# Kernel tuning notes

Hardware: AMD Instinct MI355X
Metric: run time of the kernel (lower is better)

The kernel has to match this reference:

```python
import jax, jax.numpy as jnp
import numpy as np
import math

B, S, D = 2, 2048, 1024
H, KV, HD = 16, 4, 64
N_REP = H // KV
ROPE_THETA = 1.0e6


def _rope_tables(seq_len, head_dim, theta):
    inv_freq = 1.0 / (theta ** (np.arange(0, head_dim, 2, dtype=np.float32) / head_dim))
    t = np.arange(seq_len, dtype=np.float32)
    freqs = np.outer(t, inv_freq)                      # [S, HD/2]
    emb = np.concatenate([freqs, freqs], axis=-1)      # [S, HD]
    return jnp.asarray(np.cos(emb)), jnp.asarray(np.sin(emb))


def setup_inputs() -> dict:
    key = jax.random.key(0)
    ks = jax.random.split(key, 6)
    cos, sin = _rope_tables(S, HD, ROPE_THETA)
    scale = 0.02
    return {
        "x": jax.random.normal(ks[0], (B, S, D), dtype=jnp.float32),
        "cos": cos,
        "sin": sin,
        "Wq": jax.random.normal(ks[1], (D, H * HD), dtype=jnp.float32) * scale,
        "Wk": jax.random.normal(ks[2], (D, KV * HD), dtype=jnp.float32) * scale,
        "Wv": jax.random.normal(ks[3], (D, KV * HD), dtype=jnp.float32) * scale,
        "Wo": jax.random.normal(ks[4], (H * HD, D), dtype=jnp.float32) * scale,
    }


def _rotate_half(u):
    u1, u2 = u[..., : HD // 2], u[..., HD // 2 :]
    return jnp.concatenate([-u2, u1], axis=-1)


def reference(x, cos, sin, Wq, Wk, Wv, Wo):
    bsz, seq_len, _ = x.shape
    q = (x @ Wq).reshape(bsz, seq_len, H, HD)   # [B,S,H,HD]
    k = (x @ Wk).reshape(bsz, seq_len, KV, HD)  # [B,S,KV,HD]
    v = (x @ Wv).reshape(bsz, seq_len, KV, HD)

    # RoPE: cos/sin [S,HD] broadcast over batch and heads (unsqueeze_dim=1)
    c = cos[:seq_len][None, :, None, :]
    s = sin[:seq_len][None, :, None, :]
    q = q * c + _rotate_half(q) * s
    k = k * c + _rotate_half(k) * s

    # repeat_kv: expand KV heads groupwise to H heads
    k = jnp.repeat(k, N_REP, axis=2)  # [B,S,H,HD]
    v = jnp.repeat(v, N_REP, axis=2)

    q = q.transpose(0, 2, 1, 3)  # [B,H,S,HD]
    k = k.transpose(0, 2, 1, 3)
    v = v.transpose(0, 2, 1, 3)

    scores = jnp.einsum("bhqd,bhkd->bhqk", q, k) / math.sqrt(HD)
    causal = jnp.tril(jnp.ones((seq_len, seq_len), dtype=bool))
    scores = jnp.where(causal[None, None], scores, jnp.finfo(jnp.float32).min)
    probs = jax.nn.softmax(scores.astype(jnp.float32), axis=-1).astype(x.dtype)

    out = jnp.einsum("bhqk,bhkd->bhqd", probs, v)        # [B,H,S,HD]
    out = out.transpose(0, 2, 1, 3).reshape(bsz, seq_len, H * HD)
    return out @ Wo
```

## Files before the change

kernel.cpp:

```cpp
#include <hip/hip_runtime.h>

#define SS 2048
#define NH 16
#define NKV 4
#define HD 64

typedef __bf16 bf16;
typedef __bf16 bf16x8 __attribute__((ext_vector_type(8)));
typedef float f32x4 __attribute__((ext_vector_type(4)));

#define SM_SCALE 0.18033688011f

__device__ __forceinline__ void gl_lds16(const bf16* g, bf16* l) {
    __builtin_amdgcn_global_load_lds((const __attribute__((address_space(1))) void*)g,
                                     (__attribute__((address_space(3))) void*)l, 16, 0, 0);
}

__global__ __launch_bounds__(256) void prep_kernel(
    const float* __restrict__ Wq, const float* __restrict__ Wk,
    const float* __restrict__ Wv, const float* __restrict__ Wo,
    bf16* __restrict__ wqkv_t, bf16* __restrict__ wo_t)
{
    const int blk = blockIdx.x;
    const int tid = threadIdx.x;
    const float* W; bf16* Wt; int N, n0, k0;
    if (blk < 256)      { W = Wq; Wt = wqkv_t;                       N = 1024; n0 = (blk & 15) * 64;         k0 = (blk >> 4) * 64; }
    else if (blk < 320) { W = Wk; Wt = wqkv_t + (size_t)1024 * 1024; N = 256;  n0 = ((blk - 256) & 3) * 64;  k0 = ((blk - 256) >> 2) * 64; }
    else if (blk < 384) { W = Wv; Wt = wqkv_t + (size_t)1280 * 1024; N = 256;  n0 = ((blk - 320) & 3) * 64;  k0 = ((blk - 320) >> 2) * 64; }
    else                { W = Wo; Wt = wo_t;                         N = 1024; n0 = ((blk - 384) & 15) * 64; k0 = ((blk - 384) >> 4) * 64; }

    __shared__ float Ts[64][65];
    const int c = tid & 63, rr = tid >> 6;
    #pragma unroll
    for (int i = 0; i < 16; ++i) {
        const int kk = i * 4 + rr;
        Ts[kk][c] = W[(size_t)(k0 + kk) * N + n0 + c];
    }
    __syncthreads();
    #pragma unroll
    for (int i = 0; i < 16; ++i) {
        const int nn = i * 4 + rr;
        Wt[(size_t)(n0 + nn) * 1024 + k0 + c] = (bf16)Ts[c][nn];
    }
}

template<int EPI>
__global__ __launch_bounds__(256) void gemm_bt_kernel(
    const bf16* __restrict__ A, const float* __restrict__ Af,
    const bf16* __restrict__ Bt, float* __restrict__ C,
    const float* __restrict__ cosp, const float* __restrict__ sinp,
    bf16* __restrict__ qo, bf16* __restrict__ ko, bf16* __restrict__ vto,
    int M, int N, int K)
{
    __shared__ bf16 As[64 * 64];
    __shared__ bf16 Bs[128 * 64];
    const int m0 = blockIdx.x * 64, n0 = blockIdx.y * 128;
    const int tid = threadIdx.x;
    const int w = tid >> 6, lane = tid & 63, g = lane >> 4, li = lane & 15;
    const int wm = w >> 1, wn = w & 1;

    f32x4 acc[2][4];
    const f32x4 z = {0.f, 0.f, 0.f, 0.f};
    #pragma unroll
    for (int i = 0; i < 2; ++i)
        #pragma unroll
        for (int j = 0; j < 4; ++j) acc[i][j] = z;

    const int srow = tid >> 3;
    const int schunk = ((tid & 7) ^ (srow & 7)) * 8;
    const bf16* pB0 = Bt + (size_t)(n0 + srow) * K + schunk;
    const bf16* pB1 = Bt + (size_t)(n0 + 32 + srow) * K + schunk;
    const bf16* pB2 = Bt + (size_t)(n0 + 64 + srow) * K + schunk;
    const bf16* pB3 = Bt + (size_t)(n0 + 96 + srow) * K + schunk;
    bf16* lB0 = Bs + (size_t)w * 512;
    bf16* lB1 = Bs + 2048 + (size_t)w * 512;
    bf16* lB2 = Bs + 4096 + (size_t)w * 512;
    bf16* lB3 = Bs + 6144 + (size_t)w * 512;
    const bf16* pA0 = (EPI == 0) ? A + (size_t)(m0 + srow) * K + schunk : nullptr;
    const bf16* pA1 = (EPI == 0) ? A + (size_t)(m0 + 32 + srow) * K + schunk : nullptr;
    bf16* lA0 = As + (size_t)w * 512;
    bf16* lA1 = As + 2048 + (size_t)w * 512;

    for (int kk = 0; kk < K; kk += 64) {
        __syncthreads();
        if (EPI == 0) {
            gl_lds16(pA0 + kk, lA0);
            gl_lds16(pA1 + kk, lA1);
        } else {
            #pragma unroll
            for (int s = 0; s < 2; ++s) {
                const float* src = Af + (size_t)(m0 + s * 32 + srow) * K + kk + (tid & 7) * 8;
                const float4 v0 = *(const float4*)src;
                const float4 v1 = *(const float4*)(src + 4);
                bf16x8 t8;
                t8[0] = (bf16)v0.x; t8[1] = (bf16)v0.y; t8[2] = (bf16)v0.z; t8[3] = (bf16)v0.w;
                t8[4] = (bf16)v1.x; t8[5] = (bf16)v1.y; t8[6] = (bf16)v1.z; t8[7] = (bf16)v1.w;
                *(bf16x8*)&As[(s * 32 + srow) * 64 + schunk] = t8;
            }
        }
        gl_lds16(pB0 + kk, lB0);
        gl_lds16(pB1 + kk, lB1);
        gl_lds16(pB2 + kk, lB2);
        gl_lds16(pB3 + kk, lB3);
        __syncthreads();
        #pragma unroll
        for (int t = 0; t < 2; ++t) {
            const int phys = ((t * 4 + g) ^ (li & 7)) * 8;
            bf16x8 af[2], bfr[4];
            #pragma unroll
            for (int mi = 0; mi < 2; ++mi) af[mi] = *(const bf16x8*)&As[(wm * 32 + mi * 16 + li) * 64 + phys];
            #pragma unroll
            for (int ni = 0; ni < 4; ++ni) bfr[ni] = *(const bf16x8*)&Bs[(wn * 64 + ni * 16 + li) * 64 + phys];
            #pragma unroll
            for (int mi = 0; mi < 2; ++mi)
                #pragma unroll
                for (int ni = 0; ni < 4; ++ni)
                    acc[mi][ni] = __builtin_amdgcn_mfma_f32_16x16x32_bf16(af[mi], bfr[ni], acc[mi][ni], 0, 0, 0);
        }
    }

    const int row0 = m0 + wm * 32, col0 = n0 + wn * 64;
    if (EPI == 0) {
        #pragma unroll
        for (int mi = 0; mi < 2; ++mi)
            #pragma unroll
            for (int ni = 0; ni < 4; ++ni)
                #pragma unroll
                for (int r = 0; r < 4; ++r)
                    C[(size_t)(row0 + mi * 16 + g * 4 + r) * N + col0 + ni * 16 + li] = acc[mi][ni][r];
    } else {
        #pragma unroll
        for (int ni = 0; ni < 4; ++ni) {
            const int col = col0 + ni * 16 + li;
            const int d = col & 63;
            #pragma unroll
            for (int mi = 0; mi < 2; ++mi) {
                #pragma unroll
                for (int r = 0; r < 4; ++r) {
                    const int row = row0 + mi * 16 + g * 4 + r;
                    const int bb = row >> 11, s = row & 2047;
                    float val = acc[mi][ni][r];
                    if (col < 1280) {
                        const float pairv = acc[mi][ni ^ 2][r];
                        const float rot = (d < 32) ? -pairv : pairv;
                        val = val * cosp[s * 64 + d] + rot * sinp[s * 64 + d];
                    }
                    if (col < 1024) {
                        const int hh = col >> 6;
                        qo[(((size_t)bb * NH + hh) * SS + s) * HD + d] = (bf16)(val * SM_SCALE);
                    } else if (col < 1280) {
                        const int kh = (col - 1024) >> 6;
                        ko[(((size_t)bb * NKV + kh) * SS + s) * HD + d] = (bf16)val;
                    } else {
                        const int kh = (col - 1280) >> 6;
                        vto[(((size_t)bb * NKV + kh) * HD + d) * SS + s] = (bf16)val;
                    }
                }
            }
        }
    }
}

__global__ __launch_bounds__(256) void flash_kernel(const bf16* __restrict__ q, const bf16* __restrict__ k,
                                                    const bf16* __restrict__ vt, bf16* __restrict__ o)
{
    __shared__ bf16 Ks[128 * 64];
    __shared__ bf16 Vt[64 * 128];
    __shared__ bf16 Ps[4][16][72];

    const int blk = blockIdx.x;
    const int qt = 31 - (blk >> 5);
    const int h = blk & 15;
    const int b = (blk >> 4) & 1;
    const int kvh = h >> 2;
    const int tid = threadIdx.x;
    const int w = tid >> 6, lane = tid & 63, g = lane >> 4, li = lane & 15;

    const bf16* qh = q + ((size_t)b * NH + h) * SS * HD;
    const bf16* kh = k + ((size_t)b * NKV + kvh) * SS * HD;
    const bf16* vh = vt + ((size_t)b * NKV + kvh) * (size_t)HD * SS;

    bf16x8 ones;
    #pragma unroll
    for (int j = 0; j < 8; ++j) ones[j] = (bf16)1.0f;
    const f32x4 z = {0.f, 0.f, 0.f, 0.f};

    const bf16* qrow = qh + (size_t)(qt * 64 + w * 16 + li) * HD;
    bf16x8 qf[2];
    qf[0] = *(const bf16x8*)(qrow + g * 8);
    qf[1] = *(const bf16x8*)(qrow + 32 + g * 8);

    const int ksrow = tid >> 3;
    const int kchunk = ((tid & 7) ^ (ksrow & 7)) * 8;
    const int vsrow = tid >> 4;
    const int vchunk = (((tid & 15) ^ (vsrow & 7)) & 15) * 8;
    bf16* lK = Ks + (size_t)w * 512;
    bf16* lV = Vt + (size_t)w * 512;

    f32x4 o_acc[4], l_acc;
    #pragma unroll
    for (int nt = 0; nt < 4; ++nt) o_acc[nt] = z;
    l_acc = z;

    for (int kt0 = 0; kt0 <= qt; kt0 += 2) {
        __syncthreads();
        {
            #pragma unroll
            for (int s = 0; s < 4; ++s)
                gl_lds16(kh + (size_t)(kt0 * 64 + s * 32 + ksrow) * HD + kchunk, lK + s * 2048);
            #pragma unroll
            for (int s = 0; s < 4; ++s)
                gl_lds16(vh + (size_t)(s * 16 + vsrow) * SS + kt0 * 64 + vchunk, lV + s * 2048);
        }
        __syncthreads();

        #pragma unroll
        for (int sub = 0; sub < 2; ++sub) {
            const int kt = kt0 + sub;
            if (kt > qt) break;

            f32x4 s_acc[4];
            #pragma unroll
            for (int nt = 0; nt < 4; ++nt) s_acc[nt] = z;
            #pragma unroll
            for (int t = 0; t < 2; ++t)
                #pragma unroll
                for (int nt = 0; nt < 4; ++nt) {
                    const bf16x8 kf = *(const bf16x8*)&Ks[(sub * 64 + nt * 16 + li) * 64 + (((t * 4 + g) ^ (li & 7)) * 8)];
                    s_acc[nt] = __builtin_amdgcn_mfma_f32_16x16x32_bf16(qf[t], kf, s_acc[nt], 0, 0, 0);
                }

            if (kt == qt) {
                const int qr0 = qt * 64 + w * 16 + g * 4;
                #pragma unroll
                for (int nt = 0; nt < 4; ++nt) {
                    const int key = kt * 64 + nt * 16 + li;
                    #pragma unroll
                    for (int r = 0; r < 4; ++r) {
                        float sv = s_acc[nt][r];
                        if (key > qr0 + r) sv = -1e30f;
                        Ps[w][g * 4 + r][(nt * 16 + li) ^ (g * 16)] = (bf16)exp2f(sv);
                    }
                }
            } else {
                #pragma unroll
                for (int nt = 0; nt < 4; ++nt)
                    #pragma unroll
                    for (int r = 0; r < 4; ++r)
                        Ps[w][g * 4 + r][(nt * 16 + li) ^ (g * 16)] = (bf16)exp2f(s_acc[nt][r]);
            }

            #pragma unroll
            for (int t = 0; t < 2; ++t) {
                const bf16x8 pf = *(const bf16x8*)&Ps[w][li][(t * 32 + g * 8) ^ ((li >> 2) * 16)];
                l_acc = __builtin_amdgcn_mfma_f32_16x16x32_bf16(pf, ones, l_acc, 0, 0, 0);
                #pragma unroll
                for (int nt = 0; nt < 4; ++nt) {
                    const bf16x8 vf = *(const bf16x8*)&Vt[(nt * 16 + li) * 128 + (((sub * 8 + t * 4 + g) ^ (li & 7)) * 8)];
                    o_acc[nt] = __builtin_amdgcn_mfma_f32_16x16x32_bf16(pf, vf, o_acc[nt], 0, 0, 0);
                }
            }
        }
    }

    #pragma unroll
    for (int r = 0; r < 4; ++r) {
        const float inv = 1.f / l_acc[r];
        const int s = qt * 64 + w * 16 + g * 4 + r;
        bf16* orow = o + (((size_t)b * SS + s) * NH + h) * HD;
        #pragma unroll
        for (int nt = 0; nt < 4; ++nt) orow[nt * 16 + li] = (bf16)(o_acc[nt][r] * inv);
    }
}

extern "C" void kernel_launch(void* const* d_in, const int* in_sizes, int n_in,
                              void* d_out, int out_size, void* d_ws, size_t ws_size,
                              hipStream_t stream) {
    const float* x     = (const float*)d_in[0];
    const float* cos_t = (const float*)d_in[1];
    const float* sin_t = (const float*)d_in[2];
    const float* Wq    = (const float*)d_in[3];
    const float* Wk    = (const float*)d_in[4];
    const float* Wv    = (const float*)d_in[5];
    const float* Wo    = (const float*)d_in[6];
    float* out = (float*)d_out;

    char* wsb = (char*)d_ws;
    bf16* o_b    = (bf16*)(wsb);
    bf16* wqkv_t = (bf16*)(wsb + 8388608);
    bf16* wo_t   = (bf16*)(wsb + 11534336);
    bf16* q_b    = (bf16*)(wsb + 13631488);
    bf16* k_b    = (bf16*)(wsb + 22020096);
    bf16* vt_b   = (bf16*)(wsb + 24117248);

    prep_kernel<<<640, 256, 0, stream>>>(Wq, Wk, Wv, Wo, wqkv_t, wo_t);

    gemm_bt_kernel<2><<<dim3(64, 12), 256, 0, stream>>>(nullptr, x, wqkv_t, nullptr, cos_t, sin_t,
                                                        q_b, k_b, vt_b, 4096, 1536, 1024);
    flash_kernel<<<1024, 256, 0, stream>>>(q_b, k_b, vt_b, o_b);
    gemm_bt_kernel<0><<<dim3(64, 8), 256, 0, stream>>>(o_b, nullptr, wo_t, out, nullptr, nullptr,
                                                       nullptr, nullptr, nullptr, 4096, 1024, 1024);
}
```

Baseline: 167.2 us.

## Double flash query tile per wave and remap GEMM blocks by XCD

The flash kernel now processes 128 query rows per block, 32 per wave as two 16-row MFMA tiles. Each loaded K/V tile and K fragment is reused across both tiles, and the grid halves to 512 blocks. Masking and skip logic are recomputed per wave so each wave stops at its own causal frontier, which may leave some waves idle while others finish. The GEMM kernels switch to a 1D grid whose block index is remapped so consecutive M tiles land on the same XCD, aiming for better L2 reuse of the A and B panels.

```diff
diff --git a/kernel.cpp b/kernel.cpp
--- a/kernel.cpp
+++ b/kernel.cpp
@@ -54,7 +54,10 @@
 {
     __shared__ bf16 As[64 * 64];
     __shared__ bf16 Bs[128 * 64];
-    const int m0 = blockIdx.x * 64, n0 = blockIdx.y * 128;
+    const int nbc = N >> 7;
+    const int xcd = blockIdx.x & 7, kidx = blockIdx.x >> 3;
+    const int mb = xcd * 8 + kidx / nbc, nb = kidx % nbc;
+    const int m0 = mb * 64, n0 = nb * 128;
     const int tid = threadIdx.x;
     const int w = tid >> 6, lane = tid & 63, g = lane >> 4, li = lane & 15;
     const int wm = w >> 1, wn = w & 1;
@@ -166,15 +169,16 @@
 {
     __shared__ bf16 Ks[128 * 64];
     __shared__ bf16 Vt[64 * 128];
-    __shared__ bf16 Ps[4][16][72];
+    __shared__ bf16 Ps[4][32][72];
 
     const int blk = blockIdx.x;
-    const int qt = 31 - (blk >> 5);
+    const int qt = 15 - (blk >> 5);
     const int h = blk & 15;
     const int b = (blk >> 4) & 1;
     const int kvh = h >> 2;
     const int tid = threadIdx.x;
     const int w = tid >> 6, lane = tid & 63, g = lane >> 4, li = lane & 15;
+    const int qr_base = qt * 128 + w * 32;
 
     const bf16* qh = q + ((size_t)b * NH + h) * SS * HD;
     const bf16* kh = k + ((size_t)b * NKV + kvh) * SS * HD;
@@ -185,10 +189,13 @@
     for (int j = 0; j < 8; ++j) ones[j] = (bf16)1.0f;
     const f32x4 z = {0.f, 0.f, 0.f, 0.f};
 
-    const bf16* qrow = qh + (size_t)(qt * 64 + w * 16 + li) * HD;
-    bf16x8 qf[2];
-    qf[0] = *(const bf16x8*)(qrow + g * 8);
-    qf[1] = *(const bf16x8*)(qrow + 32 + g * 8);
+    bf16x8 qf[2][2];
+    #pragma unroll
+    for (int m = 0; m < 2; ++m) {
+        const bf16* qrow = qh + (size_t)(qr_base + m * 16 + li) * HD;
+        qf[m][0] = *(const bf16x8*)(qrow + g * 8);
+        qf[m][1] = *(const bf16x8*)(qrow + 32 + g * 8);
+    }
 
     const int ksrow = tid >> 3;
     const int kchunk = ((tid & 7) ^ (ksrow & 7)) * 8;
@@ -197,12 +204,16 @@
     bf16* lK = Ks + (size_t)w * 512;
     bf16* lV = Vt + (size_t)w * 512;
 
-    f32x4 o_acc[4], l_acc;
-    #pragma unroll
-    for (int nt = 0; nt < 4; ++nt) o_acc[nt] = z;
-    l_acc = z;
-
-    for (int kt0 = 0; kt0 <= qt; kt0 += 2) {
+    f32x4 o_acc[2][4], l_acc[2];
+    #pragma unroll
+    for (int m = 0; m < 2; ++m) {
+        l_acc[m] = z;
+        #pragma unroll
+        for (int nt = 0; nt < 4; ++nt) o_acc[m][nt] = z;
+    }
+
+    const int nsteps = 2 * qt + 2;
+    for (int kt0 = 0; kt0 < nsteps; kt0 += 2) {
         __syncthreads();
         {
             #pragma unroll
@@ -217,60 +228,75 @@
         #pragma unroll
         for (int sub = 0; sub < 2; ++sub) {
             const int kt = kt0 + sub;
-            if (kt > qt) break;
-
-            f32x4 s_acc[4];
-            #pragma unroll
-            for (int nt = 0; nt < 4; ++nt) s_acc[nt] = z;
+            if (kt * 64 > qr_base + 31) continue;
+
+            f32x4 s_acc[2][4];
+            #pragma unroll
+            for (int m = 0; m < 2; ++m)
+                #pragma unroll
+                for (int nt = 0; nt < 4; ++nt) s_acc[m][nt] = z;
             #pragma unroll
             for (int t = 0; t < 2; ++t)
                 #pragma unroll
                 for (int nt = 0; nt < 4; ++nt) {
                     const bf16x8 kf = *(const bf16x8*)&Ks[(sub * 64 + nt * 16 + li) * 64 + (((t * 4 + g) ^ (li & 7)) * 8)];
-                    s_acc[nt] = __builtin_amdgcn_mfma_f32_16x16x32_bf16(qf[t], kf, s_acc[nt], 0, 0, 0);
+                    #pragma unroll
+                    for (int m = 0; m < 2; ++m)
+                        s_acc[m][nt] = __builtin_amdgcn_mfma_f32_16x16x32_bf16(qf[m][t], kf, s_acc[m][nt], 0, 0, 0);
                 }
 
-            if (kt == qt) {
-                const int qr0 = qt * 64 + w * 16 + g * 4;
-                #pragma unroll
-                for (int nt = 0; nt < 4; ++nt) {
-                    const int key = kt * 64 + nt * 16 + li;
+            if (kt * 64 + 63 > qr_base) {
+                #pragma unroll
+                for (int m = 0; m < 2; ++m)
                     #pragma unroll
-                    for (int r = 0; r < 4; ++r) {
-                        float sv = s_acc[nt][r];
-                        if (key > qr0 + r) sv = -1e30f;
-                        Ps[w][g * 4 + r][(nt * 16 + li) ^ (g * 16)] = (bf16)exp2f(sv);
+                    for (int nt = 0; nt < 4; ++nt) {
+                        const int key = kt * 64 + nt * 16 + li;
+                        #pragma unroll
+                        for (int r = 0; r < 4; ++r) {
+                            float sv = s_acc[m][nt][r];
+                            if (key > qr_base + m * 16 + g * 4 + r) sv = -1e30f;
+                            Ps[w][m * 16 + g * 4 + r][(nt * 16 + li) ^ (g * 16)] = (bf16)exp2f(sv);
+                        }
                     }
+            } else {
+                #pragma unroll
+                for (int m = 0; m < 2; ++m)
+                    #pragma unroll
+                    for (int nt = 0; nt < 4; ++nt)
+                        #pragma unroll
+                        for (int r = 0; r < 4; ++r)
+                            Ps[w][m * 16 + g * 4 + r][(nt * 16 + li) ^ (g * 16)] = (bf16)exp2f(s_acc[m][nt][r]);
+            }
+
+            #pragma unroll
+            for (int t = 0; t < 2; ++t) {
+                bf16x8 pf[2];
+                #pragma unroll
+                for (int m = 0; m < 2; ++m) {
+                    pf[m] = *(const bf16x8*)&Ps[w][m * 16 + li][(t * 32 + g * 8) ^ ((li >> 2) * 16)];
+                    l_acc[m] = __builtin_amdgcn_mfma_f32_16x16x32_bf16(pf[m], ones, l_acc[m], 0, 0, 0);
                 }
-            } else {
-                #pragma unroll
-                for (int nt = 0; nt < 4; ++nt)
-                    #pragma unroll
-                    for (int r = 0; r < 4; ++r)
-                        Ps[w][g * 4 + r][(nt * 16 + li) ^ (g * 16)] = (bf16)exp2f(s_acc[nt][r]);
-            }
-
-            #pragma unroll
-            for (int t = 0; t < 2; ++t) {
-                const bf16x8 pf = *(const bf16x8*)&Ps[w][li][(t * 32 + g * 8) ^ ((li >> 2) * 16)];
-                l_acc = __builtin_amdgcn_mfma_f32_16x16x32_bf16(pf, ones, l_acc, 0, 0, 0);
                 #pragma unroll
                 for (int nt = 0; nt < 4; ++nt) {
                     const bf16x8 vf = *(const bf16x8*)&Vt[(nt * 16 + li) * 128 + (((sub * 8 + t * 4 + g) ^ (li & 7)) * 8)];
-                    o_acc[nt] = __builtin_amdgcn_mfma_f32_16x16x32_bf16(pf, vf, o_acc[nt], 0, 0, 0);
+                    #pragma unroll
+                    for (int m = 0; m < 2; ++m)
+                        o_acc[m][nt] = __builtin_amdgcn_mfma_f32_16x16x32_bf16(pf[m], vf, o_acc[m][nt], 0, 0, 0);
                 }
             }
         }
     }
 
     #pragma unroll
-    for (int r = 0; r < 4; ++r) {
-        const float inv = 1.f / l_acc[r];
-        const int s = qt * 64 + w * 16 + g * 4 + r;
-        bf16* orow = o + (((size_t)b * SS + s) * NH + h) * HD;
-        #pragma unroll
-        for (int nt = 0; nt < 4; ++nt) orow[nt * 16 + li] = (bf16)(o_acc[nt][r] * inv);
-    }
+    for (int m = 0; m < 2; ++m)
+        #pragma unroll
+        for (int r = 0; r < 4; ++r) {
+            const float inv = 1.f / l_acc[m][r];
+            const int s = qr_base + m * 16 + g * 4 + r;
+            bf16* orow = o + (((size_t)b * SS + s) * NH + h) * HD;
+            #pragma unroll
+            for (int nt = 0; nt < 4; ++nt) orow[nt * 16 + li] = (bf16)(o_acc[m][nt][r] * inv);
+        }
 }
 
 extern "C" void kernel_launch(void* const* d_in, const int* in_sizes, int n_in,
@@ -295,9 +321,9 @@
 
     prep_kernel<<<640, 256, 0, stream>>>(Wq, Wk, Wv, Wo, wqkv_t, wo_t);
 
-    gemm_bt_kernel<2><<<dim3(64, 12), 256, 0, stream>>>(nullptr, x, wqkv_t, nullptr, cos_t, sin_t,
-                                                        q_b, k_b, vt_b, 4096, 1536, 1024);
-    flash_kernel<<<1024, 256, 0, stream>>>(q_b, k_b, vt_b, o_b);
-    gemm_bt_kernel<0><<<dim3(64, 8), 256, 0, stream>>>(o_b, nullptr, wo_t, out, nullptr, nullptr,
-                                                       nullptr, nullptr, nullptr, 4096, 1024, 1024);
-}
+    gemm_bt_kernel<2><<<768, 256, 0, stream>>>(nullptr, x, wqkv_t, nullptr, cos_t, sin_t,
+                                               q_b, k_b, vt_b, 4096, 1536, 1024);
+    flash_kernel<<<512, 256, 0, stream>>>(q_b, k_b, vt_b, o_b);
+    gemm_bt_kernel<0><<<512, 256, 0, stream>>>(o_b, nullptr, wo_t, out, nullptr, nullptr,
+                                               nullptr, nullptr, nullptr, 4096, 1024, 1024);
+}
```

Result: slower. 181.2 us (+8.4%).
